# Kernel optimization log

Measured on AMD Instinct MI355X. Metric: run time of the kernel, lower is better.

The kernel has to match this reference:

```python
import jax, jax.numpy as jnp
import numpy as np

DIM = 512

def setup_inputs() -> dict:
    key = jax.random.key(0)
    ks = jax.random.split(key, 7)
    B, Nq, Nkv = 8, 1024, 4096
    prototype = jax.random.normal(ks[0], (B, Nq, DIM), dtype=jnp.float32)
    q_x = jax.random.normal(ks[1], (B, Nkv, DIM), dtype=jnp.float32)
    qry_attn_mask = jax.random.bernoulli(ks[2], 0.5, (B, Nkv))  # True = keep
    # Linear(dim, dim, bias=False) weights, torch convention y = x @ W.T
    s = 1.0 / np.sqrt(DIM)
    Wq = jax.random.uniform(ks[3], (DIM, DIM), jnp.float32, -s, s)
    Wk = jax.random.uniform(ks[4], (DIM, DIM), jnp.float32, -s, s)
    Wv = jax.random.uniform(ks[5], (DIM, DIM), jnp.float32, -s, s)
    Wproj = jax.random.uniform(ks[6], (DIM, DIM), jnp.float32, -s, s)
    return {"prototype": prototype, "q_x": q_x, "qry_attn_mask": qry_attn_mask,
            "Wq": Wq, "Wk": Wk, "Wv": Wv, "Wproj": Wproj}

def reference(prototype, q_x, qry_attn_mask, Wq, Wk, Wv, Wproj):
    scale = DIM ** (-0.5)
    q = jnp.einsum('bnd,ed->bne', prototype, Wq)          # [B,Nq,D]
    k = jnp.einsum('bmd,ed->bme', q_x, Wk)                # [B,Nkv,D]
    v = jnp.einsum('bmd,ed->bme', q_x, Wv)                # [B,Nkv,D]
    attn = jnp.einsum('bnd,bmd->bnm', q, k) * scale       # [B,Nq,Nkv]
    bias = (~qry_attn_mask).astype(attn.dtype)[:, None, :] * -10000.0
    attn = jax.nn.softmax(attn + bias, axis=-1)
    x = jnp.einsum('bnm,bmd->bnd', attn, v)
    x = jnp.einsum('bnd,ed->bne', x, Wproj)
    return x
```

## Files before the change

### kernel.cpp

```cpp
#include <hip/hip_runtime.h>
#include <hip/hip_bf16.h>
#include <stdint.h>


typedef __bf16 bf16;
typedef bf16 bf16x8 __attribute__((ext_vector_type(8)));
typedef bf16 bf16x4 __attribute__((ext_vector_type(4)));
typedef float f32x4 __attribute__((ext_vector_type(4)));

#define NB 8
#define NQ 1024
#define NKV 4096
#define DD 512

__device__ __forceinline__ void direct16(const void* g, void* s) {
  __builtin_amdgcn_global_load_lds(
      (const __attribute__((address_space(1))) void*)g,
      (__attribute__((address_space(3))) void*)s, 16, 0, 0);
}

__global__ void cvt_kernel(const float* __restrict__ src, bf16* __restrict__ dst, int n4) {
  int i = blockIdx.x * blockDim.x + threadIdx.x;
  if (i < n4) {
    float4 v = ((const float4*)src)[i];
    bf16x4 o;
    o.x = (bf16)v.x; o.y = (bf16)v.y; o.z = (bf16)v.z; o.w = (bf16)v.w;
    ((bf16x4*)dst)[i] = o;
  }
}

__global__ void cvt_weights(const float* __restrict__ Wq, const float* __restrict__ Wk,
                            const float* __restrict__ Wv, const float* __restrict__ Wp,
                            bf16* __restrict__ Wq_b, bf16* __restrict__ Wkv_b,
                            bf16* __restrict__ Wp_b) {
  int i = blockIdx.x * blockDim.x + threadIdx.x;
  int w = i >> 16, r = i & 65535;
  const float* src = (w == 0) ? Wq : (w == 1) ? Wk : (w == 2) ? Wv : Wp;
  bf16x4* dst = (w == 0) ? (bf16x4*)Wq_b
              : (w == 3) ? (bf16x4*)Wp_b
                         : (bf16x4*)Wkv_b + (w == 2 ? 65536 : 0);
  float4 v = ((const float4*)src)[r];
  bf16x4 o;
  o.x = (bf16)v.x; o.y = (bf16)v.y; o.z = (bf16)v.z; o.w = (bf16)v.w;
  dst[r] = o;
}

__global__ void sniff_zero(const unsigned* __restrict__ mask, int* __restrict__ flag,
                           float* __restrict__ denom) {
  __shared__ int s_bad0, s_bad1;
  if (threadIdx.x == 0) { s_bad0 = 0; s_bad1 = 0; }
  __syncthreads();
  int b0 = 0, b1 = 0;
  for (int i = threadIdx.x; i < 8192; i += 256) {
    unsigned v = mask[i];
    if (v > 1u) b0 = 1;
    if (v != 0u && v != 0x3F800000u) b1 = 1;
  }
  if (b0) atomicOr(&s_bad0, 1);
  if (b1) atomicOr(&s_bad1, 1);
  for (int i = threadIdx.x; i < NB * NQ; i += 256) denom[i] = 0.f;
  __syncthreads();
  if (threadIdx.x == 0) *flag = (s_bad0 == 0) ? 0 : ((s_bad1 == 0) ? 1 : 2);
}

__global__ void reduce_pv(const float4* __restrict__ p0, const float4* __restrict__ p1,
                          const float* __restrict__ denom, bf16x4* __restrict__ x, int n4) {
  int i = blockIdx.x * blockDim.x + threadIdx.x;
  if (i < n4) {
    float4 a = p0[i], c = p1[i];
    const float inv = 1.0f / denom[i >> 7];
    bf16x4 o;
    o.x = (bf16)((a.x + c.x) * inv); o.y = (bf16)((a.y + c.y) * inv);
    o.z = (bf16)((a.z + c.z) * inv); o.w = (bf16)((a.w + c.w) * inv);
    x[i] = o;
  }
}

template <int EPI>
__global__ void __launch_bounds__(256, 2)
gemm_bt(const bf16* __restrict__ A, const bf16* __restrict__ Bw,
        void* __restrict__ Cp, void* __restrict__ Cp2,
        int N, int Klen, int Kstride, long kOff,
        long sA, long sB, long sC,
        const void* __restrict__ mask, const int* __restrict__ flagP,
        float* __restrict__ denom, float scale, int M) {
  __shared__ alignas(16) bf16 As[128 * 32];
  __shared__ alignas(16) bf16 Bs[128 * 32];
  const int tid = threadIdx.x;
  const int wave = tid >> 6, lane = tid & 63;
  const int l15 = lane & 15, l4 = lane >> 4;
  const int wm = (wave >> 1) * 64, wn = (wave & 1) * 64;
  const int b = blockIdx.z & 7;
  const int chunk = blockIdx.z >> 3;

  const bf16* Ab = A + (long)b * sA + chunk * kOff + (long)(blockIdx.y * 128) * Kstride;
  const bf16* Bb = Bw + (long)b * sB + chunk * kOff + (long)(blockIdx.x * 128) * Kstride;

  const int c0 = wave * 2, c1 = wave * 2 + 1;
  const int srow = lane >> 2;
  const int scol = (lane & 3) * 8;
  const bf16* ag0 = Ab + (long)(c0 * 16 + srow) * Kstride + scol;
  const bf16* ag1 = Ab + (long)(c1 * 16 + srow) * Kstride + scol;
  const bf16* bg0 = Bb + (long)(c0 * 16 + srow) * Kstride + scol;
  const bf16* bg1 = Bb + (long)(c1 * 16 + srow) * Kstride + scol;
  bf16* al0 = As + c0 * 512 + lane * 8;
  bf16* al1 = As + c1 * 512 + lane * 8;
  bf16* bl0 = Bs + c0 * 512 + lane * 8;
  bf16* bl1 = Bs + c1 * 512 + lane * 8;

  f32x4 acc[4][4] = {};

  for (int kt = 0; kt < Klen; kt += 32) {
    __syncthreads();
    direct16(ag0, al0);
    direct16(ag1, al1);
    direct16(bg0, bl0);
    direct16(bg1, bl1);
    ag0 += 32; ag1 += 32; bg0 += 32; bg1 += 32;
    __syncthreads();
    bf16x8 af[4], bfr[4];
#pragma unroll
    for (int t = 0; t < 4; ++t)
      af[t] = *(const bf16x8*)(As + (wm + t * 16 + l15) * 32 + l4 * 8);
#pragma unroll
    for (int t = 0; t < 4; ++t)
      bfr[t] = *(const bf16x8*)(Bs + (wn + t * 16 + l15) * 32 + l4 * 8);
#pragma unroll
    for (int mt = 0; mt < 4; ++mt)
#pragma unroll
      for (int nt = 0; nt < 4; ++nt)
        acc[mt][nt] = __builtin_amdgcn_mfma_f32_16x16x32_bf16(af[mt], bfr[nt],
                                                              acc[mt][nt], 0, 0, 0);
  }

  const int rowBase = blockIdx.y * 128 + wm;
  const int colBase = blockIdx.x * 128 + wn;

  if constexpr (EPI == 0) {
    bf16* C = (bf16*)Cp + (long)b * sC;
#pragma unroll
    for (int mt = 0; mt < 4; ++mt)
#pragma unroll
      for (int nt = 0; nt < 4; ++nt)
#pragma unroll
        for (int r = 0; r < 4; ++r)
          C[(long)(rowBase + mt * 16 + l4 * 4 + r) * N + colBase + nt * 16 + l15] =
              (bf16)acc[mt][nt][r];
  } else if constexpr (EPI == 2) {
    bf16* C = (bf16*)Cp + (long)b * sC;
    const int mode = *flagP;
    float rs[4][4];
#pragma unroll
    for (int mt = 0; mt < 4; ++mt)
#pragma unroll
      for (int r = 0; r < 4; ++r) rs[mt][r] = 0.f;
#pragma unroll
    for (int nt = 0; nt < 4; ++nt) {
      const int col = colBase + nt * 16 + l15;
      bool keep;
      if (mode == 0)      keep = ((const int*)mask)[b * NKV + col] != 0;
      else if (mode == 1) keep = ((const float*)mask)[b * NKV + col] != 0.f;
      else                keep = ((const unsigned char*)mask)[b * NKV + col] != 0;
#pragma unroll
      for (int mt = 0; mt < 4; ++mt)
#pragma unroll
        for (int r = 0; r < 4; ++r) {
          float p = keep ? __expf(acc[mt][nt][r] * scale) : 0.f;
          rs[mt][r] += p;
          C[(long)(rowBase + mt * 16 + l4 * 4 + r) * N + col] = (bf16)p;
        }
    }
#pragma unroll
    for (int mt = 0; mt < 4; ++mt)
#pragma unroll
      for (int r = 0; r < 4; ++r) {
        float v = rs[mt][r];
        v += __shfl_xor(v, 1, 64);
        v += __shfl_xor(v, 2, 64);
        v += __shfl_xor(v, 4, 64);
        v += __shfl_xor(v, 8, 64);
        if (l15 == 0)
          atomicAdd(&denom[b * M + rowBase + mt * 16 + l4 * 4 + r], v);
      }
  } else if constexpr (EPI == 4) {
    float* C = (float*)Cp + (long)blockIdx.z * sC;
#pragma unroll
    for (int mt = 0; mt < 4; ++mt)
#pragma unroll
      for (int nt = 0; nt < 4; ++nt)
#pragma unroll
        for (int r = 0; r < 4; ++r)
          C[(long)(rowBase + mt * 16 + l4 * 4 + r) * N + colBase + nt * 16 + l15] =
              acc[mt][nt][r];
  } else {
    if (colBase < 512) {
      bf16* C = (bf16*)Cp;
#pragma unroll
      for (int mt = 0; mt < 4; ++mt)
#pragma unroll
        for (int nt = 0; nt < 4; ++nt)
#pragma unroll
          for (int r = 0; r < 4; ++r)
            C[(long)(rowBase + mt * 16 + l4 * 4 + r) * 512 + colBase + nt * 16 + l15] =
                (bf16)acc[mt][nt][r];
    } else {
      bf16* C = (bf16*)Cp2;
#pragma unroll
      for (int mt = 0; mt < 4; ++mt) {
        const int gm = rowBase + mt * 16 + l4 * 4;
        const int bb = gm >> 12, mloc = gm & 4095;
#pragma unroll
        for (int nt = 0; nt < 4; ++nt) {
          const int col = colBase + nt * 16 + l15 - 512;
          bf16x4 o;
          o.x = (bf16)acc[mt][nt][0]; o.y = (bf16)acc[mt][nt][1];
          o.z = (bf16)acc[mt][nt][2]; o.w = (bf16)acc[mt][nt][3];
          *(bf16x4*)(C + (long)bb * DD * NKV + (long)col * NKV + mloc) = o;
        }
      }
    }
  }
}

extern "C" void kernel_launch(void* const* d_in, const int* in_sizes, int n_in,
                              void* d_out, int out_size, void* d_ws, size_t ws_size,
                              hipStream_t stream) {
  const float* proto = (const float*)d_in[0];
  const float* qx    = (const float*)d_in[1];
  const void*  mask  = d_in[2];
  const float* Wq    = (const float*)d_in[3];
  const float* Wk    = (const float*)d_in[4];
  const float* Wv    = (const float*)d_in[5];
  const float* Wproj = (const float*)d_in[6];
  float* out = (float*)d_out;

  char* w = (char*)d_ws;
  int*   flag  = (int*)w;
  float* denom = (float*)(w + 4096);
  size_t off = 65536;
  bf16* Wq_b  = (bf16*)(w + off); off += (size_t)DD * DD * 2;
  bf16* Wkv_b = (bf16*)(w + off); off += (size_t)DD * DD * 4;
  bf16* Wp_b  = (bf16*)(w + off); off += (size_t)DD * DD * 2;
  bf16* q_b   = (bf16*)(w + off); off += (size_t)NB * NQ * DD * 2;
  bf16* k_b   = (bf16*)(w + off); off += (size_t)NB * NKV * DD * 2;
  float* part = (float*)k_b;
  bf16* vT_b  = (bf16*)(w + off); off += (size_t)NB * NKV * DD * 2;
  bf16* x_b   = (bf16*)(w + off); off += (size_t)NB * NQ * DD * 2;
  size_t off_pp = off;
  bf16* proto_b = (bf16*)(w + off); off += (size_t)NB * NQ * DD * 2;
  bf16* qx_b    = (bf16*)(w + off);
  bf16* P       = (bf16*)(w + off_pp);

  sniff_zero<<<1, 256, 0, stream>>>((const unsigned*)mask, flag, denom);

  cvt_kernel<<<NB * NQ * DD / 4 / 256, 256, 0, stream>>>(proto, proto_b, NB * NQ * DD / 4);
  cvt_kernel<<<NB * NKV * DD / 4 / 256, 256, 0, stream>>>(qx, qx_b, NB * NKV * DD / 4);
  cvt_weights<<<4 * 65536 / 256, 256, 0, stream>>>(Wq, Wk, Wv, Wproj, Wq_b, Wkv_b, Wp_b);

  const float scale = 0.04419417382415922f;

  gemm_bt<0><<<dim3(4, 64, 1), 256, 0, stream>>>(
      proto_b, Wq_b, q_b, nullptr, DD, DD, DD, 0L, 0L, 0L, 0L,
      nullptr, nullptr, nullptr, 0.f, 0);
  gemm_bt<5><<<dim3(8, 256, 1), 256, 0, stream>>>(
      qx_b, Wkv_b, k_b, vT_b, 1024, DD, DD, 0L, 0L, 0L, 0L,
      nullptr, nullptr, nullptr, 0.f, 0);
  gemm_bt<2><<<dim3(NKV / 128, NQ / 128, NB), 256, 0, stream>>>(
      q_b, k_b, P, nullptr, NKV, DD, DD, 0L,
      (long)NQ * DD, (long)NKV * DD, (long)NQ * NKV,
      mask, flag, denom, scale, NQ);
  gemm_bt<4><<<dim3(4, 8, 16), 256, 0, stream>>>(
      P, vT_b, part, nullptr, DD, NKV / 2, NKV, (long)NKV / 2,
      (long)NQ * NKV, (long)DD * NKV, (long)NQ * DD,
      nullptr, nullptr, nullptr, 0.f, 0);
  reduce_pv<<<NB * NQ * DD / 4 / 256, 256, 0, stream>>>(
      (const float4*)part, (const float4*)(part + (size_t)NB * NQ * DD),
      denom, (bf16x4*)x_b, NB * NQ * DD / 4);
  gemm_bt<4><<<dim3(4, 64, 1), 256, 0, stream>>>(
      x_b, Wp_b, out, nullptr, DD, DD, DD, 0L, 0L, 0L, 0L,
      nullptr, nullptr, nullptr, 0.f, 0);
}
```

Before: 368.8 us.

## Stage GEMM epilogues through LDS and add wide-tile split-K PV kernel

The bf16 GEMM epilogues (Q projection, K/V projection with V transpose, and the softmax-numerator P output) now write their tile to a padded LDS buffer and then emit coalesced 16-byte row stores, replacing scattered 2-byte and strided stores. A new pv_kernel computes P·V with 512-thread blocks covering the full 512-wide D dimension, so each P tile is loaded once instead of four times. When the workspace is large enough it splits K four ways into extra partial buffers, and reduce_pv sums them. The cost is more LDS per block (which may lower occupancy), more partial-sum memory traffic with four chunks, and a dependence on ws_size.

```diff
diff --git a/kernel.cpp b/kernel.cpp
--- a/kernel.cpp
+++ b/kernel.cpp
@@ -12,6 +12,7 @@
 #define NQ 1024
 #define NKV 4096
 #define DD 512
+#define RT_LD 136
 
 __device__ __forceinline__ void direct16(const void* g, void* s) {
   __builtin_amdgcn_global_load_lds(
@@ -63,15 +64,22 @@
   if (threadIdx.x == 0) *flag = (s_bad0 == 0) ? 0 : ((s_bad1 == 0) ? 1 : 2);
 }
 
-__global__ void reduce_pv(const float4* __restrict__ p0, const float4* __restrict__ p1,
-                          const float* __restrict__ denom, bf16x4* __restrict__ x, int n4) {
+__global__ void reduce_pv(const float4* __restrict__ p01, const float4* __restrict__ p23,
+                          const float* __restrict__ denom, bf16x4* __restrict__ x,
+                          int n4, int nchunk) {
   int i = blockIdx.x * blockDim.x + threadIdx.x;
   if (i < n4) {
-    float4 a = p0[i], c = p1[i];
+    const int S = NB * NQ * DD / 4;
+    float4 a = p01[i], c = p01[i + S];
+    float sx = a.x + c.x, sy = a.y + c.y, sz = a.z + c.z, sw = a.w + c.w;
+    if (nchunk == 4) {
+      float4 e = p23[i], f = p23[i + S];
+      sx += e.x + f.x; sy += e.y + f.y; sz += e.z + f.z; sw += e.w + f.w;
+    }
     const float inv = 1.0f / denom[i >> 7];
     bf16x4 o;
-    o.x = (bf16)((a.x + c.x) * inv); o.y = (bf16)((a.y + c.y) * inv);
-    o.z = (bf16)((a.z + c.z) * inv); o.w = (bf16)((a.w + c.w) * inv);
+    o.x = (bf16)(sx * inv); o.y = (bf16)(sy * inv);
+    o.z = (bf16)(sz * inv); o.w = (bf16)(sw * inv);
     x[i] = o;
   }
 }
@@ -80,7 +88,7 @@
 __global__ void __launch_bounds__(256, 2)
 gemm_bt(const bf16* __restrict__ A, const bf16* __restrict__ Bw,
         void* __restrict__ Cp, void* __restrict__ Cp2,
-        int N, int Klen, int Kstride, long kOff,
+        int N, int Klen, int Kstride,
         long sA, long sB, long sC,
         const void* __restrict__ mask, const int* __restrict__ flagP,
         float* __restrict__ denom, float scale, int M) {
@@ -90,11 +98,10 @@
   const int wave = tid >> 6, lane = tid & 63;
   const int l15 = lane & 15, l4 = lane >> 4;
   const int wm = (wave >> 1) * 64, wn = (wave & 1) * 64;
-  const int b = blockIdx.z & 7;
-  const int chunk = blockIdx.z >> 3;
-
-  const bf16* Ab = A + (long)b * sA + chunk * kOff + (long)(blockIdx.y * 128) * Kstride;
-  const bf16* Bb = Bw + (long)b * sB + chunk * kOff + (long)(blockIdx.x * 128) * Kstride;
+  const int b = blockIdx.z;
+
+  const bf16* Ab = A + (long)b * sA + (long)(blockIdx.y * 128) * Kstride;
+  const bf16* Bb = Bw + (long)b * sB + (long)(blockIdx.x * 128) * Kstride;
 
   const int c0 = wave * 2, c1 = wave * 2 + 1;
   const int srow = lane >> 2;
@@ -135,52 +142,65 @@
 
   const int rowBase = blockIdx.y * 128 + wm;
   const int colBase = blockIdx.x * 128 + wn;
-
-  if constexpr (EPI == 0) {
+  const int tR = blockIdx.y * 128;
+  const int tC = blockIdx.x * 128;
+
+  if constexpr (EPI == 0 || EPI == 2) {
+    __shared__ bf16 Rt[128 * RT_LD];
     bf16* C = (bf16*)Cp + (long)b * sC;
-#pragma unroll
-    for (int mt = 0; mt < 4; ++mt)
-#pragma unroll
-      for (int nt = 0; nt < 4; ++nt)
-#pragma unroll
-        for (int r = 0; r < 4; ++r)
-          C[(long)(rowBase + mt * 16 + l4 * 4 + r) * N + colBase + nt * 16 + l15] =
-              (bf16)acc[mt][nt][r];
-  } else if constexpr (EPI == 2) {
-    bf16* C = (bf16*)Cp + (long)b * sC;
-    const int mode = *flagP;
-    float rs[4][4];
-#pragma unroll
-    for (int mt = 0; mt < 4; ++mt)
-#pragma unroll
-      for (int r = 0; r < 4; ++r) rs[mt][r] = 0.f;
-#pragma unroll
-    for (int nt = 0; nt < 4; ++nt) {
-      const int col = colBase + nt * 16 + l15;
-      bool keep;
-      if (mode == 0)      keep = ((const int*)mask)[b * NKV + col] != 0;
-      else if (mode == 1) keep = ((const float*)mask)[b * NKV + col] != 0.f;
-      else                keep = ((const unsigned char*)mask)[b * NKV + col] != 0;
+    if constexpr (EPI == 0) {
 #pragma unroll
       for (int mt = 0; mt < 4; ++mt)
 #pragma unroll
+        for (int nt = 0; nt < 4; ++nt)
+#pragma unroll
+          for (int r = 0; r < 4; ++r)
+            Rt[(wm + mt * 16 + l4 * 4 + r) * RT_LD + wn + nt * 16 + l15] =
+                (bf16)acc[mt][nt][r];
+    } else {
+      const int mode = *flagP;
+      float rs[4][4];
+#pragma unroll
+      for (int mt = 0; mt < 4; ++mt)
+#pragma unroll
+        for (int r = 0; r < 4; ++r) rs[mt][r] = 0.f;
+#pragma unroll
+      for (int nt = 0; nt < 4; ++nt) {
+        const int col = colBase + nt * 16 + l15;
+        bool keep;
+        if (mode == 0)      keep = ((const int*)mask)[b * NKV + col] != 0;
+        else if (mode == 1) keep = ((const float*)mask)[b * NKV + col] != 0.f;
+        else                keep = ((const unsigned char*)mask)[b * NKV + col] != 0;
+#pragma unroll
+        for (int mt = 0; mt < 4; ++mt)
+#pragma unroll
+          for (int r = 0; r < 4; ++r) {
+            float p = keep ? __expf(acc[mt][nt][r] * scale) : 0.f;
+            rs[mt][r] += p;
+            Rt[(wm + mt * 16 + l4 * 4 + r) * RT_LD + wn + nt * 16 + l15] = (bf16)p;
+          }
+      }
+#pragma unroll
+      for (int mt = 0; mt < 4; ++mt)
+#pragma unroll
         for (int r = 0; r < 4; ++r) {
-          float p = keep ? __expf(acc[mt][nt][r] * scale) : 0.f;
-          rs[mt][r] += p;
-          C[(long)(rowBase + mt * 16 + l4 * 4 + r) * N + col] = (bf16)p;
+          float v = rs[mt][r];
+          v += __shfl_xor(v, 1, 64);
+          v += __shfl_xor(v, 2, 64);
+          v += __shfl_xor(v, 4, 64);
+          v += __shfl_xor(v, 8, 64);
+          if (l15 == 0)
+            atomicAdd(&denom[b * M + rowBase + mt * 16 + l4 * 4 + r], v);
         }
     }
-#pragma unroll
-    for (int mt = 0; mt < 4; ++mt)
-#pragma unroll
-      for (int r = 0; r < 4; ++r) {
-        float v = rs[mt][r];
-        v += __shfl_xor(v, 1, 64);
-        v += __shfl_xor(v, 2, 64);
-        v += __shfl_xor(v, 4, 64);
-        v += __shfl_xor(v, 8, 64);
-        if (l15 == 0)
-          atomicAdd(&denom[b * M + rowBase + mt * 16 + l4 * 4 + r], v);
+    __syncthreads();
+    const int r0 = tid >> 2, cq = (tid & 3) * 32;
+#pragma unroll
+    for (int h = 0; h < 128; h += 64)
+#pragma unroll
+      for (int j = 0; j < 4; ++j) {
+        bf16x8 v = *(const bf16x8*)(Rt + (r0 + h) * RT_LD + cq + j * 8);
+        *(bf16x8*)(C + (long)(tR + r0 + h) * N + tC + cq + j * 8) = v;
       }
   } else if constexpr (EPI == 4) {
     float* C = (float*)Cp + (long)blockIdx.z * sC;
@@ -193,7 +213,8 @@
           C[(long)(rowBase + mt * 16 + l4 * 4 + r) * N + colBase + nt * 16 + l15] =
               acc[mt][nt][r];
   } else {
-    if (colBase < 512) {
+    if (tC < 512) {
+      __shared__ bf16 Rt[128 * RT_LD];
       bf16* C = (bf16*)Cp;
 #pragma unroll
       for (int mt = 0; mt < 4; ++mt)
@@ -201,25 +222,104 @@
         for (int nt = 0; nt < 4; ++nt)
 #pragma unroll
           for (int r = 0; r < 4; ++r)
-            C[(long)(rowBase + mt * 16 + l4 * 4 + r) * 512 + colBase + nt * 16 + l15] =
+            Rt[(wm + mt * 16 + l4 * 4 + r) * RT_LD + wn + nt * 16 + l15] =
                 (bf16)acc[mt][nt][r];
+      __syncthreads();
+      const int r0 = tid >> 2, cq = (tid & 3) * 32;
+#pragma unroll
+      for (int h = 0; h < 128; h += 64)
+#pragma unroll
+        for (int j = 0; j < 4; ++j) {
+          bf16x8 v = *(const bf16x8*)(Rt + (r0 + h) * RT_LD + cq + j * 8);
+          *(bf16x8*)(C + (long)(tR + r0 + h) * 512 + tC + cq + j * 8) = v;
+        }
     } else {
+      __shared__ bf16 Rt[128 * RT_LD];
       bf16* C = (bf16*)Cp2;
 #pragma unroll
       for (int mt = 0; mt < 4; ++mt) {
-        const int gm = rowBase + mt * 16 + l4 * 4;
-        const int bb = gm >> 12, mloc = gm & 4095;
+        const int r0 = wm + mt * 16 + l4 * 4;
 #pragma unroll
         for (int nt = 0; nt < 4; ++nt) {
-          const int col = colBase + nt * 16 + l15 - 512;
+          const int cloc = wn + nt * 16 + l15;
           bf16x4 o;
           o.x = (bf16)acc[mt][nt][0]; o.y = (bf16)acc[mt][nt][1];
           o.z = (bf16)acc[mt][nt][2]; o.w = (bf16)acc[mt][nt][3];
-          *(bf16x4*)(C + (long)bb * DD * NKV + (long)col * NKV + mloc) = o;
+          *(bf16x4*)(Rt + cloc * RT_LD + r0) = o;
         }
       }
+      __syncthreads();
+      const int bb = tR >> 12, kvloc = tR & 4095;
+      const int d0 = tid >> 2, kvq = (tid & 3) * 32;
+#pragma unroll
+      for (int h = 0; h < 128; h += 64)
+#pragma unroll
+        for (int j = 0; j < 4; ++j) {
+          bf16x8 v = *(const bf16x8*)(Rt + (d0 + h) * RT_LD + kvq + j * 8);
+          *(bf16x8*)(C + (long)bb * DD * NKV + (long)(tC - 512 + d0 + h) * NKV +
+                     kvloc + kvq + j * 8) = v;
+        }
     }
   }
+}
+
+__global__ void __launch_bounds__(512, 2)
+pv_kernel(const bf16* __restrict__ P, const bf16* __restrict__ vT,
+          float* __restrict__ partA, float* __restrict__ partB, int Klen) {
+  __shared__ alignas(16) bf16 As[128 * 32];
+  __shared__ alignas(16) bf16 Bs[512 * 32];
+  const int tid = threadIdx.x;
+  const int wave = tid >> 6, lane = tid & 63;
+  const int l15 = lane & 15, l4 = lane >> 4;
+  const int wm = (wave >> 2) * 64, wn = (wave & 3) * 128;
+  const int b = blockIdx.z & 7;
+  const int chunk = blockIdx.z >> 3;
+  const int yB = blockIdx.y * 128;
+
+  const bf16* Ab = P + (long)b * NQ * NKV + (long)chunk * Klen;
+  const bf16* Bb = vT + (long)b * DD * NKV + (long)chunk * Klen;
+
+  const int srow = lane >> 2, scol = (lane & 3) * 8;
+  const bf16* ag = Ab + (long)(yB + wave * 16 + srow) * NKV + scol;
+  bf16* al = As + wave * 512 + lane * 8;
+  const bf16* bg0 = Bb + (long)(wave * 64 + srow) * NKV + scol;
+  bf16* bl = Bs + wave * 2048 + lane * 8;
+
+  f32x4 acc[4][8] = {};
+
+  for (int kt = 0; kt < Klen; kt += 32) {
+    __syncthreads();
+    direct16(ag, al);
+#pragma unroll
+    for (int c = 0; c < 4; ++c)
+      direct16(bg0 + (long)c * 16 * NKV, bl + c * 512);
+    ag += 32; bg0 += 32;
+    __syncthreads();
+    bf16x8 af[4], bfr[8];
+#pragma unroll
+    for (int t = 0; t < 4; ++t)
+      af[t] = *(const bf16x8*)(As + (wm + t * 16 + l15) * 32 + l4 * 8);
+#pragma unroll
+    for (int t = 0; t < 8; ++t)
+      bfr[t] = *(const bf16x8*)(Bs + (wn + t * 16 + l15) * 32 + l4 * 8);
+#pragma unroll
+    for (int mt = 0; mt < 4; ++mt)
+#pragma unroll
+      for (int nt = 0; nt < 8; ++nt)
+        acc[mt][nt] = __builtin_amdgcn_mfma_f32_16x16x32_bf16(af[mt], bfr[nt],
+                                                              acc[mt][nt], 0, 0, 0);
+  }
+
+  float* C = ((chunk < 2) ? partA : partB) +
+             (long)(chunk & 1) * NB * NQ * DD + (long)b * NQ * DD;
+#pragma unroll
+  for (int mt = 0; mt < 4; ++mt)
+#pragma unroll
+    for (int nt = 0; nt < 8; ++nt)
+#pragma unroll
+      for (int r = 0; r < 4; ++r)
+        C[(long)(yB + wm + mt * 16 + l4 * 4 + r) * DD + wn + nt * 16 + l15] =
+            acc[mt][nt][r];
 }
 
 extern "C" void kernel_launch(void* const* d_in, const int* in_sizes, int n_in,
@@ -243,13 +343,24 @@
   bf16* Wp_b  = (bf16*)(w + off); off += (size_t)DD * DD * 2;
   bf16* q_b   = (bf16*)(w + off); off += (size_t)NB * NQ * DD * 2;
   bf16* k_b   = (bf16*)(w + off); off += (size_t)NB * NKV * DD * 2;
-  float* part = (float*)k_b;
   bf16* vT_b  = (bf16*)(w + off); off += (size_t)NB * NKV * DD * 2;
   bf16* x_b   = (bf16*)(w + off); off += (size_t)NB * NQ * DD * 2;
   size_t off_pp = off;
   bf16* proto_b = (bf16*)(w + off); off += (size_t)NB * NQ * DD * 2;
-  bf16* qx_b    = (bf16*)(w + off);
+  bf16* qx_b    = (bf16*)(w + off); off += (size_t)NB * NKV * DD * 4;
   bf16* P       = (bf16*)(w + off_pp);
+  const size_t slab = (size_t)NB * NQ * DD * 4;
+  int nchunk;
+  float *partA, *partB;
+  if (ws_size >= off + 4 * slab) {
+    nchunk = 4;
+    partA = (float*)(w + off);
+    partB = (float*)(w + off + 2 * slab);
+  } else {
+    nchunk = 2;
+    partA = (float*)k_b;
+    partB = (float*)k_b;
+  }
 
   sniff_zero<<<1, 256, 0, stream>>>((const unsigned*)mask, flag, denom);
 
@@ -260,23 +371,21 @@
   const float scale = 0.04419417382415922f;
 
   gemm_bt<0><<<dim3(4, 64, 1), 256, 0, stream>>>(
-      proto_b, Wq_b, q_b, nullptr, DD, DD, DD, 0L, 0L, 0L, 0L,
+      proto_b, Wq_b, q_b, nullptr, DD, DD, DD, 0L, 0L, 0L,
       nullptr, nullptr, nullptr, 0.f, 0);
   gemm_bt<5><<<dim3(8, 256, 1), 256, 0, stream>>>(
-      qx_b, Wkv_b, k_b, vT_b, 1024, DD, DD, 0L, 0L, 0L, 0L,
+      qx_b, Wkv_b, k_b, vT_b, 1024, DD, DD, 0L, 0L, 0L,
       nullptr, nullptr, nullptr, 0.f, 0);
   gemm_bt<2><<<dim3(NKV / 128, NQ / 128, NB), 256, 0, stream>>>(
-      q_b, k_b, P, nullptr, NKV, DD, DD, 0L,
+      q_b, k_b, P, nullptr, NKV, DD, DD,
       (long)NQ * DD, (long)NKV * DD, (long)NQ * NKV,
       mask, flag, denom, scale, NQ);
-  gemm_bt<4><<<dim3(4, 8, 16), 256, 0, stream>>>(
-      P, vT_b, part, nullptr, DD, NKV / 2, NKV, (long)NKV / 2,
-      (long)NQ * NKV, (long)DD * NKV, (long)NQ * DD,
+  pv_kernel<<<dim3(1, NQ / 128, NB * nchunk), 512, 0, stream>>>(
+      P, vT_b, partA, partB, NKV / nchunk);
+  reduce_pv<<<NB * NQ * DD / 4 / 256, 256, 0, stream>>>(
+      (const float4*)partA, (const float4*)partB, denom, (bf16x4*)x_b,
+      NB * NQ * DD / 4, nchunk);
+  gemm_bt<4><<<dim3(4, 64, 1), 256, 0, stream>>>(
+      x_b, Wp_b, out, nullptr, DD, DD, DD, 0L, 0L, 0L,
       nullptr, nullptr, nullptr, 0.f, 0);
-  reduce_pv<<<NB * NQ * DD / 4 / 256, 256, 0, stream>>>(
-      (const float4*)part, (const float4*)(part + (size_t)NB * NQ * DD),
-      denom, (bf16x4*)x_b, NB * NQ * DD / 4);
-  gemm_bt<4><<<dim3(4, 64, 1), 256, 0, stream>>>(
-      x_b, Wp_b, out, nullptr, DD, DD, DD, 0L, 0L, 0L, 0L,
-      nullptr, nullptr, nullptr, 0.f, 0);
-}
+}
```

Result: slower. 452.9 us (+22.8%).
